# Performance work log

Hardware: AMD Instinct MI355X
Metric: run time of the kernel (lower is better)

Reference implementation:

```python
import jax, jax.numpy as jnp
import numpy as np

B, N, C = 8, 2048, 256
H = 8
D = C // H
HID = 4 * C
EPS = 1e-5


def _layernorm(x, g, b):
    m = jnp.mean(x, axis=-1, keepdims=True)
    v = jnp.mean((x - m) ** 2, axis=-1, keepdims=True)
    return (x - m) * jax.lax.rsqrt(v + EPS) * g + b


def setup_inputs() -> dict:
    key = jax.random.key(0)
    ks = jax.random.split(key, 8)
    s = 0.02
    return {
        "x": jax.random.normal(ks[0], (B, N, C), dtype=jnp.float32),
        "ln1_g": jnp.ones((C,), jnp.float32),
        "ln1_b": jnp.zeros((C,), jnp.float32),
        "qkv_w": jax.random.normal(ks[1], (3 * C, C), jnp.float32) * s,  # torch Linear: (out,in), no bias
        "scale": jnp.asarray(D ** -0.5, jnp.float32),  # learnable temperature scalar
        "proj_w": jax.random.normal(ks[2], (C, C), jnp.float32) * s,
        "proj_b": jnp.zeros((C,), jnp.float32),
        "ln2_g": jnp.ones((C,), jnp.float32),
        "ln2_b": jnp.zeros((C,), jnp.float32),
        "fc1_w": jax.random.normal(ks[3], (HID, C), jnp.float32) * s,
        "fc1_b": jnp.zeros((HID,), jnp.float32),
        "fc2_w": jax.random.normal(ks[4], (C, HID), jnp.float32) * s,
        "fc2_b": jnp.zeros((C,), jnp.float32),
    }


def _attn(x, qkv_w, scale, proj_w, proj_b):
    b, n, c = x.shape
    qkv = (x @ qkv_w.T).reshape(b, n, 3, H, D)
    qkv = jnp.transpose(qkv, (2, 0, 3, 1, 4))  # (3, B, H, N, D)
    q, k, v = qkv[0], qkv[1], qkv[2]
    attn = jnp.einsum("bhnd,bhmd->bhnm", q, k) * scale  # full NxN scores (faithful)
    eye = jnp.eye(n, dtype=bool)
    attn = jnp.where(eye, -jnp.inf, attn)  # mask diagonal (no self-relation)
    attn = jax.nn.softmax(attn, axis=-1)
    out = jnp.einsum("bhnm,bhmd->bhnd", attn, v)
    out = jnp.transpose(out, (0, 2, 1, 3)).reshape(b, n, c)
    return out @ proj_w.T + proj_b


def reference(x, ln1_g, ln1_b, qkv_w, scale, proj_w, proj_b,
              ln2_g, ln2_b, fc1_w, fc1_b, fc2_w, fc2_b):
    x = x + _attn(_layernorm(x, ln1_g, ln1_b), qkv_w, scale, proj_w, proj_b)
    h = _layernorm(x, ln2_g, ln2_b)
    h = jax.nn.gelu(h @ fc1_w.T + fc1_b, approximate=False)  # torch GELU default = exact
    x = x + (h @ fc2_w.T + fc2_b)
    return x
```

## Files before the change

kernel.cpp:

```cpp
#include <hip/hip_runtime.h>
#include <cstdint>
#include <cstddef>


typedef __bf16 bf16x8 __attribute__((ext_vector_type(8)));
typedef __bf16 bf16x4 __attribute__((ext_vector_type(4)));
typedef float  f32x4  __attribute__((ext_vector_type(4)));

#define BN_TOK   2048
#define CC       256
#define HID_DIM  1024
#define MROWS    16384

#define OFF_W    0u
#define OFF_A    1572864u
#define OFF_QKV  9961472u
#define OFF_H    35127296u
#define WOFF_QKV 0
#define WOFF_PRJ 196608
#define WOFF_FC1 262144
#define WOFF_FC2 524288

__device__ __forceinline__ void gload_lds16(const __bf16* g, __bf16* l) {
    __builtin_amdgcn_global_load_lds(
        (const __attribute__((address_space(1))) void*)g,
        (__attribute__((address_space(3))) void*)l, 16, 0, 0);
}

__global__ __launch_bounds__(256) void cvt_w_kernel(
    const float* __restrict__ q, const float* __restrict__ p,
    const float* __restrict__ f1, const float* __restrict__ f2,
    __bf16* __restrict__ dst)
{
    int i = (blockIdx.x * 256 + threadIdx.x) * 4;
    const float* src; int off;
    if (i < 196608)      { src = q;  off = 0; }
    else if (i < 262144) { src = p;  off = 196608; }
    else if (i < 524288) { src = f1; off = 262144; }
    else                 { src = f2; off = 524288; }
    float4 v = *(const float4*)(src + (i - off));
    bf16x4 o;
    o[0] = (__bf16)v.x; o[1] = (__bf16)v.y; o[2] = (__bf16)v.z; o[3] = (__bf16)v.w;
    *(bf16x4*)(dst + i) = o;
}

__global__ __launch_bounds__(256) void ln_kernel(
    const float* __restrict__ x, const float* __restrict__ g,
    const float* __restrict__ b, __bf16* __restrict__ y)
{
    const int lane = threadIdx.x & 63;
    const int row  = blockIdx.x * 4 + (threadIdx.x >> 6);
    const float4 xv = *(const float4*)(x + (size_t)row * CC + lane * 4);
    float s  = xv.x + xv.y + xv.z + xv.w;
    float s2 = xv.x*xv.x + xv.y*xv.y + xv.z*xv.z + xv.w*xv.w;
#pragma unroll
    for (int m = 1; m < 64; m <<= 1) {
        s  += __shfl_xor(s,  m);
        s2 += __shfl_xor(s2, m);
    }
    const float mean = s * (1.0f / 256.0f);
    const float var  = fmaxf(s2 * (1.0f / 256.0f) - mean * mean, 0.0f);
    const float rstd = rsqrtf(var + 1e-5f);
    const float4 gv = *(const float4*)(g + lane * 4);
    const float4 bv = *(const float4*)(b + lane * 4);
    bf16x4 o;
    o[0] = (__bf16)((xv.x - mean) * rstd * gv.x + bv.x);
    o[1] = (__bf16)((xv.y - mean) * rstd * gv.y + bv.y);
    o[2] = (__bf16)((xv.z - mean) * rstd * gv.z + bv.z);
    o[3] = (__bf16)((xv.w - mean) * rstd * gv.w + bv.w);
    *(bf16x4*)(y + (size_t)row * CC + lane * 4) = o;
}

template<int BIAS, int GELU, int RES, int OUTBF>
__global__ __launch_bounds__(256) void gemm128(
    const __bf16* __restrict__ A, const __bf16* __restrict__ W,
    const float* __restrict__ bias, const float* __restrict__ res,
    void* __restrict__ outp, int M, int N, int K)
{
    __shared__ __align__(16) __bf16 As[128 * 32];
    __shared__ __align__(16) __bf16 Bs[128 * 32];
    const int tid = threadIdx.x, lane = tid & 63, wid = tid >> 6;
    const int wr = wid >> 1, wc = wid & 1;
    const int fr = lane & 15, fg = lane >> 4;
    const int tm = blockIdx.x * 128, tn = blockIdx.y * 128;

    const int lrow = lane >> 2, lk = (lane & 3) * 8;
    const __bf16* gA = A + (size_t)(tm + wid * 32 + lrow) * K + lk;
    const __bf16* gB = W + (size_t)(tn + wid * 32 + lrow) * K + lk;
    __bf16* lA = As + wid * 1024;
    __bf16* lB = Bs + wid * 1024;
    const size_t rowK16 = (size_t)16 * K;

    f32x4 acc[4][4];
    const f32x4 vz = {0.f, 0.f, 0.f, 0.f};
#pragma unroll
    for (int mi = 0; mi < 4; ++mi)
#pragma unroll
        for (int nj = 0; nj < 4; ++nj) acc[mi][nj] = vz;

    for (int k0 = 0; k0 < K; k0 += 32) {
        gload_lds16(gA + k0,          lA);
        gload_lds16(gA + rowK16 + k0, lA + 512);
        gload_lds16(gB + k0,          lB);
        gload_lds16(gB + rowK16 + k0, lB + 512);
        __syncthreads();
        bf16x8 af[4], bfv[4];
#pragma unroll
        for (int mi = 0; mi < 4; ++mi)
            af[mi] = *(const bf16x8*)&As[(wr * 64 + mi * 16 + fr) * 32 + fg * 8];
#pragma unroll
        for (int nj = 0; nj < 4; ++nj)
            bfv[nj] = *(const bf16x8*)&Bs[(wc * 64 + nj * 16 + fr) * 32 + fg * 8];
#pragma unroll
        for (int mi = 0; mi < 4; ++mi)
#pragma unroll
            for (int nj = 0; nj < 4; ++nj)
                acc[mi][nj] = __builtin_amdgcn_mfma_f32_16x16x32_bf16(
                    af[mi], bfv[nj], acc[mi][nj], 0, 0, 0);
        __syncthreads();
    }

#pragma unroll
    for (int mi = 0; mi < 4; ++mi) {
#pragma unroll
        for (int nj = 0; nj < 4; ++nj) {
            const int col = tn + wc * 64 + nj * 16 + fr;
            float bv = 0.0f;
            if (BIAS) bv = bias[col];
#pragma unroll
            for (int r = 0; r < 4; ++r) {
                const int row = tm + wr * 64 + mi * 16 + fg * 4 + r;
                float v = acc[mi][nj][r];
                if (BIAS) v += bv;
                if (GELU) v = v * 0.5f * (1.0f + erff(v * 0.70710678118654752f));
                if (RES)  v += res[(size_t)row * N + col];
                if (OUTBF) ((__bf16*)outp)[(size_t)row * N + col] = (__bf16)v;
                else       ((float*)outp)[(size_t)row * N + col]  = v;
            }
        }
    }
}

__global__ __launch_bounds__(256) void attn_kernel(
    const __bf16* __restrict__ qkv, const float* __restrict__ scale_p,
    __bf16* __restrict__ ao)
{
    __shared__ __align__(16) __bf16 Ks[64][40];
    __shared__ __align__(16) __bf16 Vt[32][72];
    __shared__ __align__(16) unsigned char PsT[4][32 * 128];

    const int tid = threadIdx.x, lane = tid & 63, wid = tid >> 6;
    const int fr = lane & 15, fg = lane >> 4;
    const int qt = blockIdx.x;
    const int bh = blockIdx.y;
    const int b = bh >> 3, h = bh & 7;
    const float c = scale_p[0] * 1.4426950408889634f;
    const size_t base = (size_t)b * BN_TOK * 768;
    const int hq = h * 32, hk = 256 + h * 32;
    const int ib = qt * 128 + wid * 32;

    bf16x8 qf[2];
    qf[0] = *(const bf16x8*)&qkv[base + (size_t)(ib + fr) * 768 + hq + fg * 8];
    qf[1] = *(const bf16x8*)&qkv[base + (size_t)(ib + 16 + fr) * 768 + hq + fg * 8];

    const f32x4 vz = {0.f, 0.f, 0.f, 0.f};
    f32x4 accd[2][2];
    accd[0][0] = vz; accd[0][1] = vz; accd[1][0] = vz; accd[1][1] = vz;
    float psum[2] = {0.f, 0.f};

    const int sj = tid >> 2, sd = (tid & 3) * 8;
    const int eperm = (tid & 3) << 1;
    const __bf16* kptr = qkv + base + (size_t)sj * 768 + hk + sd;
    const __bf16* vptr = kptr + 256;

    unsigned char* pst = &PsT[wid][0];
    const int swz = (fr & 7) << 4;

    for (int jt = 0; jt < 32; ++jt) {
        const int jb = jt * 64;
        __syncthreads();
        *(bf16x8*)&Ks[sj][sd] = *(const bf16x8*)kptr;
        const bf16x8 vv = *(const bf16x8*)vptr;
#pragma unroll
        for (int t = 0; t < 8; ++t) {
            const int e = t ^ eperm;
            Vt[sd + e][sj] = vv[e];
        }
        kptr += (size_t)64 * 768; vptr += (size_t)64 * 768;
        __syncthreads();

        bf16x8 kf[4], vb[2][2];
#pragma unroll
        for (int nj = 0; nj < 4; ++nj)
            kf[nj] = *(const bf16x8*)&Ks[nj * 16 + fr][fg * 8];
#pragma unroll
        for (int ka = 0; ka < 2; ++ka)
#pragma unroll
            for (int dh = 0; dh < 2; ++dh)
                vb[ka][dh] = *(const bf16x8*)&Vt[dh * 16 + fr][ka * 32 + fg * 8];

        const bool dmask = (jb < ib + 32) && (ib < jb + 64);

#pragma unroll
        for (int mi = 0; mi < 2; ++mi) {
            f32x4 s[4];
#pragma unroll
            for (int nj = 0; nj < 4; ++nj)
                s[nj] = __builtin_amdgcn_mfma_f32_16x16x32_bf16(kf[nj], qf[mi], vz, 0, 0, 0);
#pragma unroll
            for (int nj = 0; nj < 4; ++nj)
#pragma unroll
                for (int r = 0; r < 4; ++r)
                    s[nj][r] = exp2f(s[nj][r] * c);
            if (dmask) {
                const int gi = ib + mi * 16 + fr;
#pragma unroll
                for (int nj = 0; nj < 4; ++nj) {
                    const int gj = jb + nj * 16 + fg * 4;
#pragma unroll
                    for (int r = 0; r < 4; ++r)
                        if (gj + r == gi) s[nj][r] = 0.f;
                }
            }
            unsigned char* pr = pst + (mi * 16 + fr) * 128;
#pragma unroll
            for (int nj = 0; nj < 4; ++nj) {
                psum[mi] += (s[nj][0] + s[nj][1]) + (s[nj][2] + s[nj][3]);
                bf16x4 pk;
                pk[0] = (__bf16)s[nj][0]; pk[1] = (__bf16)s[nj][1];
                pk[2] = (__bf16)s[nj][2]; pk[3] = (__bf16)s[nj][3];
                *(bf16x4*)(pr + ((nj * 32 + fg * 8) ^ swz)) = pk;
            }
        }
#pragma unroll
        for (int mi = 0; mi < 2; ++mi) {
            unsigned char* pr = pst + (mi * 16 + fr) * 128;
#pragma unroll
            for (int ka = 0; ka < 2; ++ka) {
                const bf16x8 pa = *(const bf16x8*)(pr + ((ka * 64 + fg * 16) ^ swz));
#pragma unroll
                for (int dh = 0; dh < 2; ++dh)
                    accd[mi][dh] = __builtin_amdgcn_mfma_f32_16x16x32_bf16(
                        pa, vb[ka][dh], accd[mi][dh], 0, 0, 0);
            }
        }
    }

#pragma unroll
    for (int mi = 0; mi < 2; ++mi) {
        float p = psum[mi];
        p += __shfl_xor(p, 16);
        p += __shfl_xor(p, 32);
        psum[mi] = p;
    }
    float rinv[2][4];
#pragma unroll
    for (int mi = 0; mi < 2; ++mi)
#pragma unroll
        for (int r = 0; r < 4; ++r)
            rinv[mi][r] = 1.0f / __shfl(psum[mi], fg * 4 + r);

#pragma unroll
    for (int mi = 0; mi < 2; ++mi)
#pragma unroll
        for (int dh = 0; dh < 2; ++dh)
#pragma unroll
            for (int r = 0; r < 4; ++r) {
                const int i = ib + mi * 16 + fg * 4 + r;
                const float o = accd[mi][dh][r] * rinv[mi][r];
                ao[(size_t)(b * BN_TOK + i) * CC + h * 32 + dh * 16 + fr] = (__bf16)o;
            }
}

extern "C" void kernel_launch(void* const* d_in, const int* in_sizes, int n_in,
                              void* d_out, int out_size, void* d_ws, size_t ws_size,
                              hipStream_t stream)
{
    const float* x      = (const float*)d_in[0];
    const float* ln1_g  = (const float*)d_in[1];
    const float* ln1_b  = (const float*)d_in[2];
    const float* qkv_w  = (const float*)d_in[3];
    const float* scale  = (const float*)d_in[4];
    const float* proj_w = (const float*)d_in[5];
    const float* proj_b = (const float*)d_in[6];
    const float* ln2_g  = (const float*)d_in[7];
    const float* ln2_b  = (const float*)d_in[8];
    const float* fc1_w  = (const float*)d_in[9];
    const float* fc1_b  = (const float*)d_in[10];
    const float* fc2_w  = (const float*)d_in[11];
    const float* fc2_b  = (const float*)d_in[12];

    char* ws = (char*)d_ws;
    __bf16* wbf   = (__bf16*)(ws + OFF_W);
    __bf16* abf   = (__bf16*)(ws + OFF_A);
    __bf16* qkvbf = (__bf16*)(ws + OFF_QKV);
    float*  x1    = (float*) (ws + OFF_QKV);
    __bf16* hbf   = (__bf16*)(ws + OFF_H);
    float*  out   = (float*)d_out;

    cvt_w_kernel<<<768, 256, 0, stream>>>(qkv_w, proj_w, fc1_w, fc2_w, wbf);
    ln_kernel<<<4096, 256, 0, stream>>>(x, ln1_g, ln1_b, abf);
    gemm128<0,0,0,1><<<dim3(128,6), 256, 0, stream>>>(
        abf, wbf + WOFF_QKV, nullptr, nullptr, qkvbf, MROWS, 768, 256);
    attn_kernel<<<dim3(16,64), 256, 0, stream>>>(qkvbf, scale, abf);
    gemm128<1,0,1,0><<<dim3(128,2), 256, 0, stream>>>(
        abf, wbf + WOFF_PRJ, proj_b, x, x1, MROWS, 256, 256);
    ln_kernel<<<4096, 256, 0, stream>>>(x1, ln2_g, ln2_b, abf);
    gemm128<1,1,0,1><<<dim3(128,8), 256, 0, stream>>>(
        abf, wbf + WOFF_FC1, fc1_b, nullptr, hbf, MROWS, HID_DIM, 256);
    gemm128<1,0,1,0><<<dim3(128,2), 256, 0, stream>>>(
        hbf, wbf + WOFF_FC2, fc2_b, x1, out, MROWS, 256, HID_DIM);
}
```

Before: 301.3 us.

## Triple-buffer GEMM and attention loads, pre-transpose V, store residual in bf16

The GEMM and attention loops now use a three-stage LDS ring fed by async global-to-LDS loads, waiting with explicit vmcnt counts and one barrier per step. The QKV GEMM epilogue writes V transposed to a separate buffer, which removes the per-tile scalar transpose in attention. Attention folds the scale into Q, computes row sums with an MFMA against ones, and uses swizzled LDS layouts. The post-attention residual x1 is stored in bf16, read back by a new bf16 layernorm, and the N=256 GEMMs use BM=64 tiles for more blocks. Storing x1 in bf16 lowers residual precision, and the hand-written waitcnt counts are fragile.

```diff
diff --git a/kernel.cpp b/kernel.cpp
--- a/kernel.cpp
+++ b/kernel.cpp
@@ -71,57 +71,130 @@
     *(bf16x4*)(y + (size_t)row * CC + lane * 4) = o;
 }
 
-template<int BIAS, int GELU, int RES, int OUTBF>
-__global__ __launch_bounds__(256) void gemm128(
+__global__ __launch_bounds__(256) void ln_bf_kernel(
+    const __bf16* __restrict__ x, const float* __restrict__ g,
+    const float* __restrict__ b, __bf16* __restrict__ y)
+{
+    const int lane = threadIdx.x & 63;
+    const int row  = blockIdx.x * 4 + (threadIdx.x >> 6);
+    const bf16x4 xv = *(const bf16x4*)&x[(size_t)row * CC + lane * 4];
+    float x0 = (float)xv[0], x1 = (float)xv[1], x2 = (float)xv[2], x3 = (float)xv[3];
+    float s  = x0 + x1 + x2 + x3;
+    float s2 = x0*x0 + x1*x1 + x2*x2 + x3*x3;
+#pragma unroll
+    for (int m = 1; m < 64; m <<= 1) {
+        s  += __shfl_xor(s,  m);
+        s2 += __shfl_xor(s2, m);
+    }
+    const float mean = s * (1.0f / 256.0f);
+    const float var  = fmaxf(s2 * (1.0f / 256.0f) - mean * mean, 0.0f);
+    const float rstd = rsqrtf(var + 1e-5f);
+    const float4 gv = *(const float4*)(g + lane * 4);
+    const float4 bv = *(const float4*)(b + lane * 4);
+    bf16x4 o;
+    o[0] = (__bf16)((x0 - mean) * rstd * gv.x + bv.x);
+    o[1] = (__bf16)((x1 - mean) * rstd * gv.y + bv.y);
+    o[2] = (__bf16)((x2 - mean) * rstd * gv.z + bv.z);
+    o[3] = (__bf16)((x3 - mean) * rstd * gv.w + bv.w);
+    *(bf16x4*)(y + (size_t)row * CC + lane * 4) = o;
+}
+
+template<int BM, int BIAS, int GELU, int RES, int RESBF, int OUTBF, int VSPLIT>
+__global__ __launch_bounds__(256) void gemm_k(
     const __bf16* __restrict__ A, const __bf16* __restrict__ W,
-    const float* __restrict__ bias, const float* __restrict__ res,
-    void* __restrict__ outp, int M, int N, int K)
-{
-    __shared__ __align__(16) __bf16 As[128 * 32];
-    __shared__ __align__(16) __bf16 Bs[128 * 32];
+    const float* __restrict__ bias, const void* __restrict__ resv,
+    void* __restrict__ outp, __bf16* __restrict__ vT, int M, int N, int K)
+{
+    constexpr int MI  = BM / 32;
+    constexpr int ASZ = BM * 32;
+    __shared__ __align__(16) __bf16 As[3 * ASZ];
+    __shared__ __align__(16) __bf16 Bs[3 * 4096];
     const int tid = threadIdx.x, lane = tid & 63, wid = tid >> 6;
     const int wr = wid >> 1, wc = wid & 1;
     const int fr = lane & 15, fg = lane >> 4;
-    const int tm = blockIdx.x * 128, tn = blockIdx.y * 128;
+    const int tm = blockIdx.x * BM, tn = blockIdx.y * 128;
 
     const int lrow = lane >> 2, lk = (lane & 3) * 8;
-    const __bf16* gA = A + (size_t)(tm + wid * 32 + lrow) * K + lk;
+    const __bf16* gA = A + (size_t)(tm + (BM == 128 ? wid * 32 : wid * 16) + lrow) * K + lk;
     const __bf16* gB = W + (size_t)(tn + wid * 32 + lrow) * K + lk;
-    __bf16* lA = As + wid * 1024;
-    __bf16* lB = Bs + wid * 1024;
     const size_t rowK16 = (size_t)16 * K;
-
-    f32x4 acc[4][4];
+    const int aoff = (BM == 128 ? wid * 1024 : wid * 512);
+    const int boff = wid * 1024;
+
+    const int KT = K >> 5;
+
+    auto STAGE = [&](int kt, int buf) {
+        const int k0 = kt * 32;
+        __bf16* lA = As + buf * ASZ + aoff;
+        __bf16* lB = Bs + buf * 4096 + boff;
+        gload_lds16(gA + k0, lA);
+        if (BM == 128) gload_lds16(gA + rowK16 + k0, lA + 512);
+        gload_lds16(gB + k0, lB);
+        gload_lds16(gB + rowK16 + k0, lB + 512);
+    };
+
+    f32x4 acc[MI][4];
     const f32x4 vz = {0.f, 0.f, 0.f, 0.f};
 #pragma unroll
-    for (int mi = 0; mi < 4; ++mi)
+    for (int mi = 0; mi < MI; ++mi)
 #pragma unroll
         for (int nj = 0; nj < 4; ++nj) acc[mi][nj] = vz;
 
-    for (int k0 = 0; k0 < K; k0 += 32) {
-        gload_lds16(gA + k0,          lA);
-        gload_lds16(gA + rowK16 + k0, lA + 512);
-        gload_lds16(gB + k0,          lB);
-        gload_lds16(gB + rowK16 + k0, lB + 512);
-        __syncthreads();
-        bf16x8 af[4], bfv[4];
-#pragma unroll
-        for (int mi = 0; mi < 4; ++mi)
-            af[mi] = *(const bf16x8*)&As[(wr * 64 + mi * 16 + fr) * 32 + fg * 8];
+    STAGE(0, 0);
+    STAGE(1 < KT ? 1 : 0, 1);
+    if (BM == 128) asm volatile("s_waitcnt vmcnt(4)" ::: "memory");
+    else           asm volatile("s_waitcnt vmcnt(3)" ::: "memory");
+    __builtin_amdgcn_s_barrier();
+
+    int cur = 0;
+    for (int k = 0; k < KT; ++k) {
+        int nt = k + 2; if (nt > KT - 1) nt = KT - 1;
+        int sb = cur + 2; if (sb >= 3) sb -= 3;
+        STAGE(nt, sb);
+
+        const __bf16* bA = As + cur * ASZ;
+        const __bf16* bB = Bs + cur * 4096;
+        bf16x8 af[MI], bfv[4];
+#pragma unroll
+        for (int mi = 0; mi < MI; ++mi)
+            af[mi] = *(const bf16x8*)&bA[(wr * (BM / 2) + mi * 16 + fr) * 32 + fg * 8];
 #pragma unroll
         for (int nj = 0; nj < 4; ++nj)
-            bfv[nj] = *(const bf16x8*)&Bs[(wc * 64 + nj * 16 + fr) * 32 + fg * 8];
-#pragma unroll
-        for (int mi = 0; mi < 4; ++mi)
+            bfv[nj] = *(const bf16x8*)&bB[(wc * 64 + nj * 16 + fr) * 32 + fg * 8];
+#pragma unroll
+        for (int mi = 0; mi < MI; ++mi)
 #pragma unroll
             for (int nj = 0; nj < 4; ++nj)
                 acc[mi][nj] = __builtin_amdgcn_mfma_f32_16x16x32_bf16(
                     af[mi], bfv[nj], acc[mi][nj], 0, 0, 0);
-        __syncthreads();
-    }
-
-#pragma unroll
-    for (int mi = 0; mi < 4; ++mi) {
+
+        if (BM == 128) asm volatile("s_waitcnt vmcnt(4)" ::: "memory");
+        else           asm volatile("s_waitcnt vmcnt(3)" ::: "memory");
+        __builtin_amdgcn_s_barrier();
+        cur += 1; if (cur == 3) cur = 0;
+    }
+    asm volatile("s_waitcnt vmcnt(0)" ::: "memory");
+
+    if (VSPLIT && tn >= 512) {
+#pragma unroll
+        for (int mi = 0; mi < MI; ++mi) {
+#pragma unroll
+            for (int nj = 0; nj < 4; ++nj) {
+                const int dfull = tn - 512 + wc * 64 + nj * 16 + fr;
+                const int row0  = tm + wr * (BM / 2) + mi * 16 + fg * 4;
+                const int bb = row0 >> 11;
+                const int n0 = row0 & 2047;
+                bf16x4 pk;
+                pk[0] = (__bf16)acc[mi][nj][0]; pk[1] = (__bf16)acc[mi][nj][1];
+                pk[2] = (__bf16)acc[mi][nj][2]; pk[3] = (__bf16)acc[mi][nj][3];
+                *(bf16x4*)&vT[((size_t)(bb * 8 + (dfull >> 5)) * 32 + (dfull & 31)) * 2048 + n0] = pk;
+            }
+        }
+        return;
+    }
+
+#pragma unroll
+    for (int mi = 0; mi < MI; ++mi) {
 #pragma unroll
         for (int nj = 0; nj < 4; ++nj) {
             const int col = tn + wc * 64 + nj * 16 + fr;
@@ -129,11 +202,14 @@
             if (BIAS) bv = bias[col];
 #pragma unroll
             for (int r = 0; r < 4; ++r) {
-                const int row = tm + wr * 64 + mi * 16 + fg * 4 + r;
+                const int row = tm + wr * (BM / 2) + mi * 16 + fg * 4 + r;
                 float v = acc[mi][nj][r];
                 if (BIAS) v += bv;
                 if (GELU) v = v * 0.5f * (1.0f + erff(v * 0.70710678118654752f));
-                if (RES)  v += res[(size_t)row * N + col];
+                if (RES) {
+                    if (RESBF) v += (float)((const __bf16*)resv)[(size_t)row * N + col];
+                    else       v += ((const float*)resv)[(size_t)row * N + col];
+                }
                 if (OUTBF) ((__bf16*)outp)[(size_t)row * N + col] = (__bf16)v;
                 else       ((float*)outp)[(size_t)row * N + col]  = v;
             }
@@ -142,12 +218,12 @@
 }
 
 __global__ __launch_bounds__(256) void attn_kernel(
-    const __bf16* __restrict__ qkv, const float* __restrict__ scale_p,
-    __bf16* __restrict__ ao)
-{
-    __shared__ __align__(16) __bf16 Ks[64][40];
-    __shared__ __align__(16) __bf16 Vt[32][72];
-    __shared__ __align__(16) unsigned char PsT[4][32 * 128];
+    const __bf16* __restrict__ qkv, const __bf16* __restrict__ vT,
+    const float* __restrict__ scale_p, __bf16* __restrict__ ao)
+{
+    __shared__ __align__(16) __bf16 Ks[3 * 2048];
+    __shared__ __align__(16) __bf16 Vs[3 * 2048];
+    __shared__ __align__(16) unsigned char PsT[4][4096];
 
     const int tid = threadIdx.x, lane = tid & 63, wid = tid >> 6;
     const int fr = lane & 15, fg = lane >> 4;
@@ -159,45 +235,63 @@
     const int hq = h * 32, hk = 256 + h * 32;
     const int ib = qt * 128 + wid * 32;
 
+    const bf16x8 q0 = *(const bf16x8*)&qkv[base + (size_t)(ib + fr) * 768 + hq + fg * 8];
+    const bf16x8 q1 = *(const bf16x8*)&qkv[base + (size_t)(ib + 16 + fr) * 768 + hq + fg * 8];
     bf16x8 qf[2];
-    qf[0] = *(const bf16x8*)&qkv[base + (size_t)(ib + fr) * 768 + hq + fg * 8];
-    qf[1] = *(const bf16x8*)&qkv[base + (size_t)(ib + 16 + fr) * 768 + hq + fg * 8];
+#pragma unroll
+    for (int e = 0; e < 8; ++e) {
+        qf[0][e] = (__bf16)((float)q0[e] * c);
+        qf[1][e] = (__bf16)((float)q1[e] * c);
+    }
+    bf16x8 onesb;
+#pragma unroll
+    for (int e = 0; e < 8; ++e) onesb[e] = (__bf16)1.0f;
 
     const f32x4 vz = {0.f, 0.f, 0.f, 0.f};
     f32x4 accd[2][2];
     accd[0][0] = vz; accd[0][1] = vz; accd[1][0] = vz; accd[1][1] = vz;
-    float psum[2] = {0.f, 0.f};
-
-    const int sj = tid >> 2, sd = (tid & 3) * 8;
-    const int eperm = (tid & 3) << 1;
-    const __bf16* kptr = qkv + base + (size_t)sj * 768 + hk + sd;
-    const __bf16* vptr = kptr + 256;
+    f32x4 accp[2]; accp[0] = vz; accp[1] = vz;
+
+    const int srow = tid >> 2;
+    const int kblk = ((tid & 3) ^ (srow & 3)) * 8;
+    const __bf16* ksrc = qkv + base + (size_t)srow * 768 + hk + kblk;
+    const int vd   = tid >> 3;
+    const int vblk = ((tid & 7) ^ (vd & 7)) * 8;
+    const __bf16* vsrc = vT + ((size_t)(bh * 32 + vd)) * 2048 + vblk;
+    __bf16* kdw = Ks + wid * 512;
+    __bf16* vdw = Vs + wid * 512;
+
+    auto STAGE = [&](int nt, int buf) {
+        gload_lds16(ksrc + (size_t)nt * 64 * 768, kdw + buf * 2048);
+        gload_lds16(vsrc + nt * 64,               vdw + buf * 2048);
+    };
 
     unsigned char* pst = &PsT[wid][0];
     const int swz = (fr & 7) << 4;
 
+    STAGE(0, 0);
+    STAGE(1, 1);
+    asm volatile("s_waitcnt vmcnt(2)" ::: "memory");
+    __builtin_amdgcn_s_barrier();
+
+    int cur = 0;
     for (int jt = 0; jt < 32; ++jt) {
         const int jb = jt * 64;
-        __syncthreads();
-        *(bf16x8*)&Ks[sj][sd] = *(const bf16x8*)kptr;
-        const bf16x8 vv = *(const bf16x8*)vptr;
-#pragma unroll
-        for (int t = 0; t < 8; ++t) {
-            const int e = t ^ eperm;
-            Vt[sd + e][sj] = vv[e];
-        }
-        kptr += (size_t)64 * 768; vptr += (size_t)64 * 768;
-        __syncthreads();
-
+        int nt = jt + 2; if (nt > 31) nt = 31;
+        int sb = cur + 2; if (sb >= 3) sb -= 3;
+        STAGE(nt, sb);
+
+        const __bf16* kb = Ks + cur * 2048;
+        const __bf16* vbuf = Vs + cur * 2048;
         bf16x8 kf[4], vb[2][2];
 #pragma unroll
         for (int nj = 0; nj < 4; ++nj)
-            kf[nj] = *(const bf16x8*)&Ks[nj * 16 + fr][fg * 8];
+            kf[nj] = *(const bf16x8*)&kb[(nj * 16 + fr) * 32 + ((fg ^ (fr & 3)) * 8)];
 #pragma unroll
         for (int ka = 0; ka < 2; ++ka)
 #pragma unroll
             for (int dh = 0; dh < 2; ++dh)
-                vb[ka][dh] = *(const bf16x8*)&Vt[dh * 16 + fr][ka * 32 + fg * 8];
+                vb[ka][dh] = *(const bf16x8*)&vbuf[(dh * 16 + fr) * 64 + (((ka * 4 + fg) ^ (fr & 7)) * 8)];
 
         const bool dmask = (jb < ib + 32) && (ib < jb + 64);
 
@@ -211,7 +305,7 @@
             for (int nj = 0; nj < 4; ++nj)
 #pragma unroll
                 for (int r = 0; r < 4; ++r)
-                    s[nj][r] = exp2f(s[nj][r] * c);
+                    s[nj][r] = exp2f(s[nj][r]);
             if (dmask) {
                 const int gi = ib + mi * 16 + fr;
 #pragma unroll
@@ -225,7 +319,6 @@
             unsigned char* pr = pst + (mi * 16 + fr) * 128;
 #pragma unroll
             for (int nj = 0; nj < 4; ++nj) {
-                psum[mi] += (s[nj][0] + s[nj][1]) + (s[nj][2] + s[nj][3]);
                 bf16x4 pk;
                 pk[0] = (__bf16)s[nj][0]; pk[1] = (__bf16)s[nj][1];
                 pk[2] = (__bf16)s[nj][2]; pk[3] = (__bf16)s[nj][3];
@@ -242,23 +335,15 @@
                 for (int dh = 0; dh < 2; ++dh)
                     accd[mi][dh] = __builtin_amdgcn_mfma_f32_16x16x32_bf16(
                         pa, vb[ka][dh], accd[mi][dh], 0, 0, 0);
+                accp[mi] = __builtin_amdgcn_mfma_f32_16x16x32_bf16(
+                    pa, onesb, accp[mi], 0, 0, 0);
             }
         }
-    }
-
-#pragma unroll
-    for (int mi = 0; mi < 2; ++mi) {
-        float p = psum[mi];
-        p += __shfl_xor(p, 16);
-        p += __shfl_xor(p, 32);
-        psum[mi] = p;
-    }
-    float rinv[2][4];
-#pragma unroll
-    for (int mi = 0; mi < 2; ++mi)
-#pragma unroll
-        for (int r = 0; r < 4; ++r)
-            rinv[mi][r] = 1.0f / __shfl(psum[mi], fg * 4 + r);
+        asm volatile("s_waitcnt vmcnt(2)" ::: "memory");
+        __builtin_amdgcn_s_barrier();
+        cur += 1; if (cur == 3) cur = 0;
+    }
+    asm volatile("s_waitcnt vmcnt(0)" ::: "memory");
 
 #pragma unroll
     for (int mi = 0; mi < 2; ++mi)
@@ -267,7 +352,7 @@
 #pragma unroll
             for (int r = 0; r < 4; ++r) {
                 const int i = ib + mi * 16 + fg * 4 + r;
-                const float o = accd[mi][dh][r] * rinv[mi][r];
+                const float o = accd[mi][dh][r] / accp[mi][r];
                 ao[(size_t)(b * BN_TOK + i) * CC + h * 32 + dh * 16 + fr] = (__bf16)o;
             }
 }
@@ -294,20 +379,21 @@
     __bf16* wbf   = (__bf16*)(ws + OFF_W);
     __bf16* abf   = (__bf16*)(ws + OFF_A);
     __bf16* qkvbf = (__bf16*)(ws + OFF_QKV);
-    float*  x1    = (float*) (ws + OFF_QKV);
+    __bf16* x1bf  = (__bf16*)(ws + OFF_QKV);
+    __bf16* vT    = (__bf16*)(ws + OFF_H);
     __bf16* hbf   = (__bf16*)(ws + OFF_H);
     float*  out   = (float*)d_out;
 
     cvt_w_kernel<<<768, 256, 0, stream>>>(qkv_w, proj_w, fc1_w, fc2_w, wbf);
     ln_kernel<<<4096, 256, 0, stream>>>(x, ln1_g, ln1_b, abf);
-    gemm128<0,0,0,1><<<dim3(128,6), 256, 0, stream>>>(
-        abf, wbf + WOFF_QKV, nullptr, nullptr, qkvbf, MROWS, 768, 256);
-    attn_kernel<<<dim3(16,64), 256, 0, stream>>>(qkvbf, scale, abf);
-    gemm128<1,0,1,0><<<dim3(128,2), 256, 0, stream>>>(
-        abf, wbf + WOFF_PRJ, proj_b, x, x1, MROWS, 256, 256);
-    ln_kernel<<<4096, 256, 0, stream>>>(x1, ln2_g, ln2_b, abf);
-    gemm128<1,1,0,1><<<dim3(128,8), 256, 0, stream>>>(
-        abf, wbf + WOFF_FC1, fc1_b, nullptr, hbf, MROWS, HID_DIM, 256);
-    gemm128<1,0,1,0><<<dim3(128,2), 256, 0, stream>>>(
-        hbf, wbf + WOFF_FC2, fc2_b, x1, out, MROWS, 256, HID_DIM);
-}
+    gemm_k<128,0,0,0,0,1,1><<<dim3(128,6), 256, 0, stream>>>(
+        abf, wbf + WOFF_QKV, nullptr, nullptr, qkvbf, vT, MROWS, 768, 256);
+    attn_kernel<<<dim3(16,64), 256, 0, stream>>>(qkvbf, vT, scale, abf);
+    gemm_k<64,1,0,1,0,1,0><<<dim3(256,2), 256, 0, stream>>>(
+        abf, wbf + WOFF_PRJ, proj_b, x, x1bf, nullptr, MROWS, 256, 256);
+    ln_bf_kernel<<<4096, 256, 0, stream>>>(x1bf, ln2_g, ln2_b, abf);
+    gemm_k<128,1,1,0,0,1,0><<<dim3(128,8), 256, 0, stream>>>(
+        abf, wbf + WOFF_FC1, fc1_b, nullptr, hbf, nullptr, MROWS, HID_DIM, 256);
+    gemm_k<64,1,0,1,1,0,0><<<dim3(256,2), 256, 0, stream>>>(
+        hbf, wbf + WOFF_FC2, fc2_b, x1bf, out, nullptr, MROWS, 256, HID_DIM);
+}
```

Measured after the change: 261.8 us. 1.15x faster.
